# Optimization experiments

Hardware: AMD Instinct MI355X
Metric: run time of the kernel (lower is better)

The kernel has to match this reference:

```python
import jax, jax.numpy as jnp
import numpy as np

# feature-map geometry: input 1024x1024, resnet50 stride 32
H_FM, W_FM = 32, 32
N_ANC = 9
SCALES = (2.0, 4.0, 6.0)
RATIOS = (0.5, 1.0, 1.5)
H_SCALE, W_SCALE = 32.0, 32.0  # input_size // backbone_hw
C_IN, HID = 2048, 512
BATCH = 8


def _anchor_grid():
    """Anchor boxes [H_FM, W_FM, 9, 4] in xyxy feature-map coords, clipped."""
    xs = jnp.arange(W_FM, dtype=jnp.float32) + 0.5
    ys = jnp.arange(H_FM, dtype=jnp.float32) + 0.5
    cx, cy = jnp.meshgrid(xs, ys)  # [H, W]
    ws, hs = [], []
    for s in SCALES:
        for r in RATIOS:
            ws.append(s * r)
            hs.append(s)
    ws = jnp.asarray(ws, jnp.float32)  # [9]
    hs = jnp.asarray(hs, jnp.float32)
    cx = cx[..., None]
    cy = cy[..., None]
    x1 = jnp.clip(cx - ws / 2, 0.0, float(W_FM))
    y1 = jnp.clip(cy - hs / 2, 0.0, float(H_FM))
    x2 = jnp.clip(cx + ws / 2, 0.0, float(W_FM))
    y2 = jnp.clip(cy + hs / 2, 0.0, float(H_FM))
    return jnp.stack([x1, y1, x2, y2], axis=-1)  # [H, W, 9, 4]


def _conv2d(x, w, b, pad):
    y = jax.lax.conv_general_dilated(
        x, w, window_strides=(1, 1), padding=[(pad, pad), (pad, pad)],
        dimension_numbers=('NCHW', 'OIHW', 'NCHW'))
    return y + b[None, :, None, None]


def setup_inputs() -> dict:
    key = jax.random.key(0)
    ks = jax.random.split(key, 4)

    def init(k, shape, fan_in):
        return jax.random.normal(k, shape, jnp.float32) * (1.0 / np.sqrt(fan_in))

    return {
        'feature_maps': jax.random.normal(ks[0], (BATCH, C_IN, H_FM, W_FM), jnp.float32),
        'hidden_w': init(ks[1], (HID, C_IN, 3, 3), C_IN * 9),
        'hidden_b': jnp.zeros((HID,), jnp.float32),
        'conf_w': init(ks[2], (N_ANC, HID, 1, 1), HID),
        'conf_b': jnp.zeros((N_ANC,), jnp.float32),
        'reg_w': init(ks[3], (N_ANC * 4, HID, 1, 1), HID),
        'reg_b': jnp.zeros((N_ANC * 4,), jnp.float32),
    }


def reference(feature_maps, hidden_w, hidden_b, conf_w, conf_b, reg_w, reg_b):
    # ProposalModule (eval mode: dropout is identity)
    x = jax.nn.relu(_conv2d(feature_maps, hidden_w, hidden_b, 1))    # [B,512,H,W]
    conf = _conv2d(x, conf_w, conf_b, 0).transpose(0, 2, 3, 1)       # [B,H,W,9]
    offs = _conv2d(x, reg_w, reg_b, 0).transpose(0, 2, 3, 1)         # [B,H,W,36]

    b = feature_maps.shape[0]
    scores = jax.nn.sigmoid(conf).reshape(b, -1)                     # [B, A]
    offs = offs.reshape(b, -1, 4)                                    # [B, A, 4]

    # apply (dxc, dyc, dw, dh) offsets to the anchor grid
    anc = _anchor_grid().reshape(-1, 4)                              # [A, 4]
    aw = anc[:, 2] - anc[:, 0]
    ah = anc[:, 3] - anc[:, 1]
    acx = anc[:, 0] + aw / 2
    acy = anc[:, 1] + ah / 2
    pcx = acx + offs[..., 0] * aw
    pcy = acy + offs[..., 1] * ah
    pw = aw * jnp.exp(offs[..., 2])
    ph = ah * jnp.exp(offs[..., 3])
    # proposals in image coordinates (xyxy)
    props = jnp.stack([
        (pcx - pw / 2) * W_SCALE,
        (pcy - ph / 2) * H_SCALE,
        (pcx + pw / 2) * W_SCALE,
        (pcy + ph / 2) * H_SCALE,
    ], axis=-1)                                                      # [B, A, 4]
    return jnp.concatenate([scores[..., None], props], axis=-1)      # [B, A, 5]
```

## Files before the change

### kernel.cpp

```cpp
#include <hip/hip_runtime.h>
#include <hip/hip_bf16.h>

typedef __attribute__((ext_vector_type(8))) short bf16x8;
typedef __attribute__((ext_vector_type(4))) float f32x4;

#define NPIX 8192
#define HIDC 512
#define CIN  2048

__device__ __forceinline__ ushort f2b(float f) {
    union { float f; unsigned u; } v; v.f = f;
    unsigned r = v.u + 0x7fffu + ((v.u >> 16) & 1u);
    return (ushort)(r >> 16);
}
__device__ __forceinline__ float b2f(ushort u) {
    union { unsigned u; float f; } v; v.u = ((unsigned)u) << 16; return v.f;
}

__device__ __forceinline__ void gload16(const void* g, void* l) {
    __builtin_amdgcn_global_load_lds(
        (const __attribute__((address_space(1))) void*)g,
        (__attribute__((address_space(3))) void*)l, 16, 0, 0);
}

#define WAITV0() asm volatile("s_waitcnt vmcnt(0)" ::: "memory")
#define BAR() do { asm volatile("s_barrier" ::: "memory"); \
                   __builtin_amdgcn_sched_barrier(0); } while (0)

__global__ void zero_border(ushort* __restrict__ xp) {
    int c = blockIdx.x;
    int b = blockIdx.y;
    int y, x;
    if (c < 34)      { y = 0;  x = c; }
    else if (c < 68) { y = 33; x = c - 34; }
    else if (c < 100){ y = c - 68 + 1; x = 0; }
    else             { y = c - 100 + 1; x = 33; }
    uint4* dst = (uint4*)(xp + (((size_t)b * 34 + y) * 34 + x) * CIN);
    uint4 z = {0u, 0u, 0u, 0u};
    dst[threadIdx.x] = z;
}

__global__ void pack_x(const float* __restrict__ x, ushort* __restrict__ xp) {
    __shared__ float tile[64][65];
    int b  = blockIdx.z;
    int c0 = blockIdx.y * 64;
    int p0 = blockIdx.x * 64;
    int t = threadIdx.x;
    int tx = t & 63, ty = t >> 6;
    const float* src = x + ((size_t)b * CIN + c0) * 1024 + p0;
    for (int i = ty; i < 64; i += 4)
        tile[i][tx] = src[(size_t)i * 1024 + tx];
    __syncthreads();
    int ci = t & 63, pj = t >> 6;
    for (int j = pj; j < 64; j += 4) {
        int p = p0 + j;
        int y = p >> 5, xx = p & 31;
        ushort* dst = xp + (((size_t)b * 34 + y + 1) * 34 + (xx + 1)) * CIN + c0;
        dst[ci] = f2b(tile[ci][j]);
    }
}

__global__ void pack_w(const float* __restrict__ hw, ushort* __restrict__ wpk) {
    __shared__ float ld[512 * 9];
    int n = blockIdx.x;
    int t = threadIdx.x;
    const float* src = hw + (size_t)n * (CIN * 9);
    for (int cc0 = 0; cc0 < CIN; cc0 += 512) {
        for (int i = t; i < 4608; i += 256) ld[i] = src[(size_t)cc0 * 9 + i];
        __syncthreads();
        for (int t9 = 0; t9 < 9; ++t9)
            for (int idx = t; idx < 512; idx += 256)
                wpk[((size_t)(t9 * 512 + n)) * CIN + cc0 + idx] = f2b(ld[idx * 9 + t9]);
        __syncthreads();
    }
}

__global__ void pack_w2(const float* __restrict__ cw, const float* __restrict__ rw,
                        ushort* __restrict__ w2b) {
    int i = blockIdx.x * 256 + threadIdx.x;
    if (i >= 48 * 512) return;
    int m = i >> 9, c = i & 511;
    float v = 0.f;
    if (m < 9) v = cw[m * 512 + c];
    else if (m < 45) v = rw[(m - 9) * 512 + c];
    w2b[i] = f2b(v);
}

#define NT_TILES 72
#define KSPLIT   4608

__launch_bounds__(512, 2)
__global__ void conv_gemm_splitk(const ushort* __restrict__ xp, const ushort* __restrict__ wpk,
                                 ushort* __restrict__ pp) {
    __shared__ __align__(16) ushort A0[256 * 64];
    __shared__ __align__(16) ushort B0[256 * 64];
    __shared__ __align__(16) ushort A1[256 * 64];
    __shared__ __align__(16) ushort B1[256 * 64];

    int t = threadIdx.x;

    int bid = blockIdx.x;
    int xcd = bid & 7;
    int nt = xcd & 1, ks = xcd >> 1;
    int mt = bid >> 3;
    int pix0 = mt * 256, n0 = nt * 256;

    int w = t >> 6, l = t & 63;
    int wr = w >> 2;
    int wc = w & 3;

    int r0 = t >> 3;
    int dOff = ((t & 7) ^ (r0 & 7)) * 8;

    int aRowBase[4];
#pragma unroll
    for (int j = 0; j < 4; ++j) {
        int p = pix0 + r0 + 64 * j;
        int b = p >> 10, py = (p >> 5) & 31, px = p & 31;
        aRowBase[j] = ((b * 34 + py) * 34 + px) * CIN;
    }
    int bRowBase[4];
#pragma unroll
    for (int j = 0; j < 4; ++j)
        bRowBase[j] = (n0 + r0 + 64 * j) * CIN;

    int ksBase = ks * KSPLIT;

    f32x4 zero = {0.f, 0.f, 0.f, 0.f};
    f32x4 acc[8][4];
#pragma unroll
    for (int i = 0; i < 8; ++i)
#pragma unroll
        for (int j = 0; j < 4; ++j) acc[i][j] = zero;

    int lr = l & 15;
    int swzA = ((l >> 4) ^ (lr & 7)) * 16;
    int swzB = ((4 + (l >> 4)) ^ (lr & 7)) * 16;
    int sz0 = (w & 1) ? swzB : swzA;
    int sz1 = (w & 1) ? swzA : swzB;
    int abase = (wr * 128 + lr) * 128;
    int bbase = (wc * 64 + lr) * 128;

    auto stageA = [&](int kt, ushort* As) {
        int fk = ksBase + kt * 64;
        int tap = fk >> 11, chc = fk & 2047;
        int dy = tap / 3, dx = tap - dy * 3;
        int aoff = (dy * 34 + dx) * CIN + chc + dOff;
#pragma unroll
        for (int j = 0; j < 4; ++j)
            gload16(xp + aRowBase[j] + aoff, (char*)As + (t + 512 * j) * 16);
    };
    auto stageB = [&](int kt, ushort* Bs) {
        int fk = ksBase + kt * 64;
        int tap = fk >> 11, chc = fk & 2047;
        int boff = tap * (512 * CIN) + chc + dOff;
#pragma unroll
        for (int j = 0; j < 4; ++j)
            gload16(wpk + bRowBase[j] + boff, (char*)Bs + (t + 512 * j) * 16);
    };

    bf16x8 a0[4], a1[4], bf0[4], bf1[4];

    auto ldA = [&](const ushort* As, int mh, int sz, bf16x8* af) {
#pragma unroll
        for (int m = 0; m < 4; ++m)
            af[m] = *(const bf16x8*)((const char*)As + abase + (mh * 4 + m) * 2048 + sz);
    };
    auto ldB = [&](const ushort* Bs, int sz, bf16x8* bf) {
#pragma unroll
        for (int ni = 0; ni < 4; ++ni)
            bf[ni] = *(const bf16x8*)((const char*)Bs + bbase + ni * 2048 + sz);
    };
    auto mm = [&](int mh, const bf16x8* af, const bf16x8* bf) {
        __builtin_amdgcn_s_setprio(1);
#pragma unroll
        for (int m = 0; m < 4; ++m)
#pragma unroll
            for (int ni = 0; ni < 4; ++ni)
                acc[mh * 4 + m][ni] = __builtin_amdgcn_mfma_f32_16x16x32_bf16(
                    af[m], bf[ni], acc[mh * 4 + m][ni], 0, 0, 0);
        __builtin_amdgcn_s_setprio(0);
    };

    auto tile = [&](int i, ushort* Ac, ushort* Bc, ushort* An, ushort* Bn) {
        bool st = (i + 1 < NT_TILES);
        WAITV0(); BAR();
        ldB(Bc, sz0, bf0);
        ldA(Ac, 0, sz0, a0);
        if (st) stageA(i + 1, An);
        mm(0, a0, bf0);
        ldA(Ac, 1, sz0, a1);
        if (st) stageB(i + 1, Bn);
        mm(1, a1, bf0);
        ldB(Bc, sz1, bf1);
        ldA(Ac, 0, sz1, a0);
        mm(0, a0, bf1);
        ldA(Ac, 1, sz1, a1);
        mm(1, a1, bf1);
    };

    stageA(0, A0); stageB(0, B0);
    for (int i = 0; i < NT_TILES; i += 2) {
        tile(i,     A0, B0, A1, B1);
        tile(i + 1, A1, B1, A0, B0);
    }

    ushort* dst = pp + (size_t)ks * (NPIX * HIDC);
    int hi = l >> 4;
#pragma unroll
    for (int mi = 0; mi < 8; ++mi) {
#pragma unroll
        for (int ni = 0; ni < 4; ++ni) {
            int col = n0 + wc * 64 + ni * 16 + lr;
#pragma unroll
            for (int r = 0; r < 4; ++r) {
                int row = pix0 + wr * 128 + mi * 16 + hi * 4 + r;
                dst[(size_t)row * HIDC + col] = f2b(acc[mi][ni][r]);
            }
        }
    }
}

#define NKSTEP 576

__launch_bounds__(256, 1)
__global__ void conv_gemm(const ushort* __restrict__ xp, const ushort* __restrict__ wpk,
                          const float* __restrict__ hb, ushort* __restrict__ hidden) {
    __shared__ __align__(16) ushort A0[128 * 32];
    __shared__ __align__(16) ushort B0[128 * 32];
    __shared__ __align__(16) ushort A1[128 * 32];
    __shared__ __align__(16) ushort B1[128 * 32];

    int t = threadIdx.x;
    int orig = blockIdx.x;
    int xcd = orig & 7;
    int ix  = orig >> 3;
    int nb  = ix & 3;
    int pb  = (xcd << 3) + (ix >> 2);
    int n0   = nb * 128;
    int pix0 = pb * 128;

    int w = t >> 6, l = t & 63;
    int wr = w >> 1, wc = w & 1;

    int u  = t ^ ((t >> 3) & 7);
    int rA = u >> 2;
    int kA = (u & 3) * 8;

    int p1 = pix0 + rA, p2 = p1 + 64;
    int b   = p1 >> 10;
    int py1 = (p1 >> 5) & 31, px1 = p1 & 31;
    int py2 = (p2 >> 5) & 31, px2 = p2 & 31;

    size_t aBase1 = ((size_t)b * 34 + py1) * 34 + px1;
    size_t aBase2 = ((size_t)b * 34 + py2) * 34 + px2;

    f32x4 zero = {0.f, 0.f, 0.f, 0.f};
    f32x4 acc[4][4];
#pragma unroll
    for (int i = 0; i < 4; ++i)
#pragma unroll
        for (int j = 0; j < 4; ++j) acc[i][j] = zero;

    int lr = l & 15;
    int kc = l >> 4;
    int sw = ((lr * 4 + kc) ^ ((lr >> 1) & 7)) * 16;

    auto stage = [&](int kk, ushort* As, ushort* Bs) {
        int tap = kk >> 6;
        int c0 = (kk & 63) << 5;
        int dy = tap / 3, dx = tap - dy * 3;
        size_t aoff = (size_t)(dy * 34 + dx) * CIN + kA + c0;
        gload16(xp + aBase1 * CIN + aoff, (char*)As + t * 16);
        gload16(xp + aBase2 * CIN + aoff, (char*)As + 4096 + t * 16);
        const ushort* bp = wpk + ((size_t)(tap * 512) + n0 + rA) * CIN + kA + c0;
        gload16(bp, (char*)Bs + t * 16);
        gload16(bp + (size_t)64 * CIN, (char*)Bs + 4096 + t * 16);
    };

    auto compute = [&](const ushort* As, const ushort* Bs) {
        const char* ab = (const char*)As + wr * 4096 + sw;
        const char* bb = (const char*)Bs + wc * 4096 + sw;
        bf16x8 af[4], bfr[4];
#pragma unroll
        for (int mi = 0; mi < 4; ++mi)
            af[mi] = *(const bf16x8*)(ab + mi * 1024);
#pragma unroll
        for (int ni = 0; ni < 4; ++ni)
            bfr[ni] = *(const bf16x8*)(bb + ni * 1024);
#pragma unroll
        for (int mi = 0; mi < 4; ++mi)
#pragma unroll
            for (int ni = 0; ni < 4; ++ni)
                acc[mi][ni] = __builtin_amdgcn_mfma_f32_16x16x32_bf16(
                    af[mi], bfr[ni], acc[mi][ni], 0, 0, 0);
    };

    stage(0, A0, B0);
    __syncthreads();
    for (int kk = 0; kk < NKSTEP; kk += 2) {
        if (kk + 1 < NKSTEP) stage(kk + 1, A1, B1);
        compute(A0, B0);
        __syncthreads();
        if (kk + 2 < NKSTEP) stage(kk + 2, A0, B0);
        compute(A1, B1);
        __syncthreads();
    }

    int lr4 = (l >> 4) * 4;
#pragma unroll
    for (int mi = 0; mi < 4; ++mi) {
#pragma unroll
        for (int ni = 0; ni < 4; ++ni) {
            int col = n0 + wc * 64 + ni * 16 + lr;
            float bias = hb[col];
#pragma unroll
            for (int r = 0; r < 4; ++r) {
                int row = pix0 + wr * 64 + mi * 16 + lr4 + r;
                float v = acc[mi][ni][r] + bias;
                v = v > 0.f ? v : 0.f;
                hidden[(size_t)row * HIDC + col] = f2b(v);
            }
        }
    }
}

__launch_bounds__(256)
__global__ void gemm2f(const ushort* __restrict__ pp, const float* __restrict__ hb,
                       const ushort* __restrict__ w2b,
                       const float* __restrict__ cb, const float* __restrict__ rb,
                       float* __restrict__ g) {
    __shared__ __align__(16) ushort W2[48 * 520];
    int t = threadIdx.x;
    const unsigned* src = (const unsigned*)w2b;
    unsigned* dstW = (unsigned*)&W2[0];
    for (int i = t; i < 12288; i += 256) {
        int m = i >> 8, c2 = i & 255;
        dstW[m * 260 + c2] = src[i];
    }
    __syncthreads();
    int w = t >> 6, l = t & 63;
    int p0 = blockIdx.x * 64 + w * 16;
    int lr = l & 15, lk = (l >> 4) * 8;
    const size_t S = (size_t)NPIX * HIDC;
    f32x4 zero = {0.f, 0.f, 0.f, 0.f};
    f32x4 acc[3] = {zero, zero, zero};
    const ushort* hrow = pp + (size_t)(p0 + lr) * HIDC + lk;
#pragma unroll 4
    for (int k0 = 0; k0 < 16; ++k0) {
        bf16x8 a0 = *(const bf16x8*)(hrow + k0 * 32);
        bf16x8 a1 = *(const bf16x8*)(hrow + S + k0 * 32);
        bf16x8 a2 = *(const bf16x8*)(hrow + 2 * S + k0 * 32);
        bf16x8 a3 = *(const bf16x8*)(hrow + 3 * S + k0 * 32);
        bf16x8 a;
#pragma unroll
        for (int j = 0; j < 8; ++j) {
            float v = b2f((ushort)a0[j]) + b2f((ushort)a1[j]) +
                      b2f((ushort)a2[j]) + b2f((ushort)a3[j]) + hb[k0 * 32 + lk + j];
            a[j] = (short)f2b(v > 0.f ? v : 0.f);
        }
#pragma unroll
        for (int ni = 0; ni < 3; ++ni) {
            bf16x8 bb = *(const bf16x8*)&W2[(ni * 16 + lr) * 520 + k0 * 32 + lk];
            acc[ni] = __builtin_amdgcn_mfma_f32_16x16x32_bf16(a, bb, acc[ni], 0, 0, 0);
        }
    }
    int lr4 = (l >> 4) * 4;
#pragma unroll
    for (int ni = 0; ni < 3; ++ni) {
        int m = ni * 16 + lr;
        float bias = (m < 9) ? cb[m] : ((m < 45) ? rb[m - 9] : 0.f);
#pragma unroll
        for (int r = 0; r < 4; ++r) {
            int p = p0 + lr4 + r;
            g[(size_t)p * 48 + m] = acc[ni][r] + bias;
        }
    }
}

__launch_bounds__(256)
__global__ void gemm2(const ushort* __restrict__ hidden, const ushort* __restrict__ w2b,
                      const float* __restrict__ cb, const float* __restrict__ rb,
                      float* __restrict__ g) {
    __shared__ __align__(16) ushort W2[48 * 520];
    int t = threadIdx.x;
    const unsigned* src = (const unsigned*)w2b;
    unsigned* dstW = (unsigned*)&W2[0];
    for (int i = t; i < 12288; i += 256) {
        int m = i >> 8, c2 = i & 255;
        dstW[m * 260 + c2] = src[i];
    }
    __syncthreads();
    int w = t >> 6, l = t & 63;
    int p0 = blockIdx.x * 64 + w * 16;
    int lr = l & 15, lk = (l >> 4) * 8;
    f32x4 zero = {0.f, 0.f, 0.f, 0.f};
    f32x4 acc[3] = {zero, zero, zero};
    const ushort* hrow = hidden + (size_t)(p0 + lr) * HIDC + lk;
#pragma unroll 4
    for (int k0 = 0; k0 < 16; ++k0) {
        bf16x8 a = *(const bf16x8*)(hrow + k0 * 32);
#pragma unroll
        for (int ni = 0; ni < 3; ++ni) {
            bf16x8 bb = *(const bf16x8*)&W2[(ni * 16 + lr) * 520 + k0 * 32 + lk];
            acc[ni] = __builtin_amdgcn_mfma_f32_16x16x32_bf16(a, bb, acc[ni], 0, 0, 0);
        }
    }
    int lr4 = (l >> 4) * 4;
#pragma unroll
    for (int ni = 0; ni < 3; ++ni) {
        int m = ni * 16 + lr;
        float bias = (m < 9) ? cb[m] : ((m < 45) ? rb[m - 9] : 0.f);
#pragma unroll
        for (int r = 0; r < 4; ++r) {
            int p = p0 + lr4 + r;
            g[(size_t)p * 48 + m] = acc[ni][r] + bias;
        }
    }
}

__global__ void proposals(const float* __restrict__ g, float* __restrict__ out) {
    int i = blockIdx.x * 256 + threadIdx.x;
    if (i >= NPIX * 9) return;
    int p = i / 9, a = i - p * 9;
    int y = (p >> 5) & 31, x = p & 31;
    int si = a / 3, ri = a - si * 3;
    float hA = 2.f * (float)(si + 1);
    float wA = (float)((si + 1) * (ri + 1));

    const float* gp = g + (size_t)p * 48;
    float conf = gp[a];
    float o0 = gp[9 + a * 4 + 0];
    float o1 = gp[9 + a * 4 + 1];
    float o2 = gp[9 + a * 4 + 2];
    float o3 = gp[9 + a * 4 + 3];

    float cx = x + 0.5f, cy = y + 0.5f;
    float x1 = fminf(fmaxf(cx - wA * 0.5f, 0.f), 32.f);
    float y1 = fminf(fmaxf(cy - hA * 0.5f, 0.f), 32.f);
    float x2 = fminf(fmaxf(cx + wA * 0.5f, 0.f), 32.f);
    float y2 = fminf(fmaxf(cy + hA * 0.5f, 0.f), 32.f);
    float aw = x2 - x1, ah = y2 - y1;
    float acx = x1 + aw * 0.5f, acy = y1 + ah * 0.5f;
    float pcx = acx + o0 * aw, pcy = acy + o1 * ah;
    float pw = aw * expf(o2), ph = ah * expf(o3);
    float s = 1.f / (1.f + expf(-conf));

    float* o = out + (size_t)i * 5;
    o[0] = s;
    o[1] = (pcx - pw * 0.5f) * 32.f;
    o[2] = (pcy - ph * 0.5f) * 32.f;
    o[3] = (pcx + pw * 0.5f) * 32.f;
    o[4] = (pcy + ph * 0.5f) * 32.f;
}

extern "C" void kernel_launch(void* const* d_in, const int* in_sizes, int n_in,
                              void* d_out, int out_size, void* d_ws, size_t ws_size,
                              hipStream_t stream) {
    const float* x  = (const float*)d_in[0];
    const float* hw = (const float*)d_in[1];
    const float* hb = (const float*)d_in[2];
    const float* cw = (const float*)d_in[3];
    const float* cb = (const float*)d_in[4];
    const float* rw = (const float*)d_in[5];
    const float* rb = (const float*)d_in[6];
    float* out = (float*)d_out;

    char* ws = (char*)d_ws;
    ushort* xp     = (ushort*)(ws);
    ushort* wpk    = (ushort*)(ws + 37879808);
    ushort* hidden = (ushort*)(ws + 56754176);
    ushort* w2b    = (ushort*)(ws + 65142784);
    float*  g      = (float*)(ws + 65191936);
    ushort* pp     = (ushort*)(ws + 66764800);
    const size_t WS_NEED_SPLITK = 66764800 + 33554432;

    hipLaunchKernelGGL(zero_border, dim3(132, 8), dim3(256), 0, stream, xp);
    hipLaunchKernelGGL(pack_x, dim3(16, 32, 8), dim3(256), 0, stream, x, xp);
    hipLaunchKernelGGL(pack_w, dim3(512), dim3(256), 0, stream, hw, wpk);
    hipLaunchKernelGGL(pack_w2, dim3(96), dim3(256), 0, stream, cw, rw, w2b);
    if (ws_size >= WS_NEED_SPLITK) {
        hipLaunchKernelGGL(conv_gemm_splitk, dim3(256), dim3(512), 0, stream, xp, wpk, pp);
        hipLaunchKernelGGL(gemm2f, dim3(128), dim3(256), 0, stream, pp, hb, w2b, cb, rb, g);
    } else {
        hipLaunchKernelGGL(conv_gemm, dim3(256), dim3(256), 0, stream, xp, wpk, hb, hidden);
        hipLaunchKernelGGL(gemm2, dim3(128), dim3(256), 0, stream, hidden, w2b, cb, rb, g);
    }
    hipLaunchKernelGGL(proposals, dim3(288), dim3(256), 0, stream, g, out);
}
```

Measured before the change: 190.5 us.

## Merge prep kernels into one launch and fuse proposal decoding into gemm2

Combines the border-zeroing, input packing, weight packing and head-weight packing kernels into a single prep kernel that dispatches on block index, removing three launches. On the split-K path it also fuses the anchor decoding, sigmoid and box computation into the second GEMM's epilogue through a shared-memory staging tile. This drops the separate proposals launch and the global round trip of the intermediate head outputs. Prep now allocates both shared buffers in every block, which may lower its occupancy.

Result: faster. 175.4 us (-7.9%).

```diff
diff --git a/kernel.cpp b/kernel.cpp
--- a/kernel.cpp
+++ b/kernel.cpp
@@ -27,63 +27,61 @@
 #define BAR() do { asm volatile("s_barrier" ::: "memory"); \
                    __builtin_amdgcn_sched_barrier(0); } while (0)
 
-__global__ void zero_border(ushort* __restrict__ xp) {
-    int c = blockIdx.x;
-    int b = blockIdx.y;
-    int y, x;
-    if (c < 34)      { y = 0;  x = c; }
-    else if (c < 68) { y = 33; x = c - 34; }
-    else if (c < 100){ y = c - 68 + 1; x = 0; }
-    else             { y = c - 100 + 1; x = 33; }
-    uint4* dst = (uint4*)(xp + (((size_t)b * 34 + y) * 34 + x) * CIN);
-    uint4 z = {0u, 0u, 0u, 0u};
-    dst[threadIdx.x] = z;
-}
-
-__global__ void pack_x(const float* __restrict__ x, ushort* __restrict__ xp) {
+__global__ void prep(const float* __restrict__ x, ushort* __restrict__ xp,
+                     const float* __restrict__ hw, ushort* __restrict__ wpk,
+                     const float* __restrict__ cw, const float* __restrict__ rw,
+                     ushort* __restrict__ w2b) {
     __shared__ float tile[64][65];
-    int b  = blockIdx.z;
-    int c0 = blockIdx.y * 64;
-    int p0 = blockIdx.x * 64;
+    __shared__ float ld[512 * 9];
+    int bid = blockIdx.x;
     int t = threadIdx.x;
-    int tx = t & 63, ty = t >> 6;
-    const float* src = x + ((size_t)b * CIN + c0) * 1024 + p0;
-    for (int i = ty; i < 64; i += 4)
-        tile[i][tx] = src[(size_t)i * 1024 + tx];
-    __syncthreads();
-    int ci = t & 63, pj = t >> 6;
-    for (int j = pj; j < 64; j += 4) {
-        int p = p0 + j;
-        int y = p >> 5, xx = p & 31;
-        ushort* dst = xp + (((size_t)b * 34 + y + 1) * 34 + (xx + 1)) * CIN + c0;
-        dst[ci] = f2b(tile[ci][j]);
-    }
-}
-
-__global__ void pack_w(const float* __restrict__ hw, ushort* __restrict__ wpk) {
-    __shared__ float ld[512 * 9];
-    int n = blockIdx.x;
-    int t = threadIdx.x;
-    const float* src = hw + (size_t)n * (CIN * 9);
-    for (int cc0 = 0; cc0 < CIN; cc0 += 512) {
-        for (int i = t; i < 4608; i += 256) ld[i] = src[(size_t)cc0 * 9 + i];
+
+    if (bid < 4096) {
+        int bx = bid & 15, by = (bid >> 4) & 31, b = bid >> 9;
+        int c0 = by * 64;
+        int p0 = bx * 64;
+        int tx = t & 63, ty = t >> 6;
+        const float* src = x + ((size_t)b * CIN + c0) * 1024 + p0;
+        for (int i = ty; i < 64; i += 4)
+            tile[i][tx] = src[(size_t)i * 1024 + tx];
         __syncthreads();
-        for (int t9 = 0; t9 < 9; ++t9)
-            for (int idx = t; idx < 512; idx += 256)
-                wpk[((size_t)(t9 * 512 + n)) * CIN + cc0 + idx] = f2b(ld[idx * 9 + t9]);
-        __syncthreads();
-    }
-}
-
-__global__ void pack_w2(const float* __restrict__ cw, const float* __restrict__ rw,
-                        ushort* __restrict__ w2b) {
-    int i = blockIdx.x * 256 + threadIdx.x;
-    if (i >= 48 * 512) return;
-    int m = i >> 9, c = i & 511;
-    float v = 0.f;
-    if (m < 9) v = cw[m * 512 + c];
-    else if (m < 45) v = rw[(m - 9) * 512 + c];
-    w2b[i] = f2b(v);
+        int ci = t & 63, pj = t >> 6;
+        for (int j = pj; j < 64; j += 4) {
+            int p = p0 + j;
+            int y = p >> 5, xx = p & 31;
+            ushort* dst = xp + (((size_t)b * 34 + y + 1) * 34 + (xx + 1)) * CIN + c0;
+            dst[ci] = f2b(tile[ci][j]);
+        }
+    } else if (bid < 4608) {
+        int n = bid - 4096;
+        const float* src = hw + (size_t)n * (CIN * 9);
+        for (int cc0 = 0; cc0 < CIN; cc0 += 512) {
+            for (int i = t; i < 4608; i += 256) ld[i] = src[(size_t)cc0 * 9 + i];
+            __syncthreads();
+            for (int t9 = 0; t9 < 9; ++t9)
+                for (int idx = t; idx < 512; idx += 256)
+                    wpk[((size_t)(t9 * 512 + n)) * CIN + cc0 + idx] = f2b(ld[idx * 9 + t9]);
+            __syncthreads();
+        }
+    } else if (bid < 4704) {
+        int i = (bid - 4608) * 256 + t;
+        int m = i >> 9, c = i & 511;
+        float v = 0.f;
+        if (m < 9) v = cw[m * 512 + c];
+        else if (m < 45) v = rw[(m - 9) * 512 + c];
+        w2b[i] = f2b(v);
+    } else {
+        int r = bid - 4704;
+        int c = r % 132, b = r / 132;
+        int y, xx;
+        if (c < 34)      { y = 0;  xx = c; }
+        else if (c < 68) { y = 33; xx = c - 34; }
+        else if (c < 100){ y = c - 68 + 1; xx = 0; }
+        else             { y = c - 100 + 1; xx = 33; }
+        uint4* dst = (uint4*)(xp + (((size_t)b * 34 + y) * 34 + xx) * CIN);
+        uint4 z = {0u, 0u, 0u, 0u};
+        dst[t] = z;
+    }
 }
 
 #define NT_TILES 72
@@ -326,11 +324,12 @@
 }
 
 __launch_bounds__(256)
-__global__ void gemm2f(const ushort* __restrict__ pp, const float* __restrict__ hb,
+__global__ void gemm2p(const ushort* __restrict__ pp, const float* __restrict__ hb,
                        const ushort* __restrict__ w2b,
                        const float* __restrict__ cb, const float* __restrict__ rb,
-                       float* __restrict__ g) {
+                       float* __restrict__ out) {
     __shared__ __align__(16) ushort W2[48 * 520];
+    __shared__ float gs[64][52];
     int t = threadIdx.x;
     const unsigned* src = (const unsigned*)w2b;
     unsigned* dstW = (unsigned*)&W2[0];
@@ -371,10 +370,43 @@
         int m = ni * 16 + lr;
         float bias = (m < 9) ? cb[m] : ((m < 45) ? rb[m - 9] : 0.f);
 #pragma unroll
-        for (int r = 0; r < 4; ++r) {
-            int p = p0 + lr4 + r;
-            g[(size_t)p * 48 + m] = acc[ni][r] + bias;
-        }
+        for (int r = 0; r < 4; ++r)
+            gs[w * 16 + lr4 + r][m] = acc[ni][r] + bias;
+    }
+    __syncthreads();
+
+    int pbase = blockIdx.x * 64;
+    for (int i = t; i < 576; i += 256) {
+        int lp = i / 9, a = i - lp * 9;
+        int p = pbase + lp;
+        int y = (p >> 5) & 31, x = p & 31;
+        int si = a / 3, ri = a - si * 3;
+        float hA = 2.f * (float)(si + 1);
+        float wA = (float)((si + 1) * (ri + 1));
+
+        float conf = gs[lp][a];
+        float o0 = gs[lp][9 + a * 4 + 0];
+        float o1 = gs[lp][9 + a * 4 + 1];
+        float o2 = gs[lp][9 + a * 4 + 2];
+        float o3 = gs[lp][9 + a * 4 + 3];
+
+        float cx = x + 0.5f, cy = y + 0.5f;
+        float x1 = fminf(fmaxf(cx - wA * 0.5f, 0.f), 32.f);
+        float y1 = fminf(fmaxf(cy - hA * 0.5f, 0.f), 32.f);
+        float x2 = fminf(fmaxf(cx + wA * 0.5f, 0.f), 32.f);
+        float y2 = fminf(fmaxf(cy + hA * 0.5f, 0.f), 32.f);
+        float aw = x2 - x1, ah = y2 - y1;
+        float acx = x1 + aw * 0.5f, acy = y1 + ah * 0.5f;
+        float pcx = acx + o0 * aw, pcy = acy + o1 * ah;
+        float pw = aw * expf(o2), ph = ah * expf(o3);
+        float s = 1.f / (1.f + expf(-conf));
+
+        float* o = out + (size_t)(p * 9 + a) * 5;
+        o[0] = s;
+        o[1] = (pcx - pw * 0.5f) * 32.f;
+        o[2] = (pcy - ph * 0.5f) * 32.f;
+        o[3] = (pcx + pw * 0.5f) * 32.f;
+        o[4] = (pcy + ph * 0.5f) * 32.f;
     }
 }
 
@@ -475,16 +507,14 @@
     ushort* pp     = (ushort*)(ws + 66764800);
     const size_t WS_NEED_SPLITK = 66764800 + 33554432;
 
-    hipLaunchKernelGGL(zero_border, dim3(132, 8), dim3(256), 0, stream, xp);
-    hipLaunchKernelGGL(pack_x, dim3(16, 32, 8), dim3(256), 0, stream, x, xp);
-    hipLaunchKernelGGL(pack_w, dim3(512), dim3(256), 0, stream, hw, wpk);
-    hipLaunchKernelGGL(pack_w2, dim3(96), dim3(256), 0, stream, cw, rw, w2b);
+    hipLaunchKernelGGL(prep, dim3(5760), dim3(256), 0, stream,
+                       x, xp, hw, wpk, cw, rw, w2b);
     if (ws_size >= WS_NEED_SPLITK) {
         hipLaunchKernelGGL(conv_gemm_splitk, dim3(256), dim3(512), 0, stream, xp, wpk, pp);
-        hipLaunchKernelGGL(gemm2f, dim3(128), dim3(256), 0, stream, pp, hb, w2b, cb, rb, g);
+        hipLaunchKernelGGL(gemm2p, dim3(128), dim3(256), 0, stream, pp, hb, w2b, cb, rb, out);
     } else {
         hipLaunchKernelGGL(conv_gemm, dim3(256), dim3(256), 0, stream, xp, wpk, hb, hidden);
         hipLaunchKernelGGL(gemm2, dim3(128), dim3(256), 0, stream, hidden, w2b, cb, rb, g);
-    }
-    hipLaunchKernelGGL(proposals, dim3(288), dim3(256), 0, stream, g, out);
-}
+        hipLaunchKernelGGL(proposals, dim3(288), dim3(256), 0, stream, g, out);
+    }
+}
```
